# Optimization experiments

Hardware: AMD Instinct MI355X
Metric: run time of the kernel (lower is better)

Reference implementation:

```python
import jax, jax.numpy as jnp
import numpy as np

B, S, HID = 2, 2048, 2048
H, KV, D = 16, 8, 128          # query heads, kv heads, head dim
NREP = H // KV
EPS = 1e-6
THETA = 1000000.0
SCALE = 1.0 / np.sqrt(D)


def setup_inputs() -> dict:
    key = jax.random.key(0)
    ks = jax.random.split(key, 5)
    x = jax.random.normal(ks[0], (B, S, HID), jnp.float32)
    std = 0.02
    Wq = jax.random.normal(ks[1], (HID, H * D), jnp.float32) * std
    Wk = jax.random.normal(ks[2], (HID, KV * D), jnp.float32) * std
    Wv = jax.random.normal(ks[3], (HID, KV * D), jnp.float32) * std
    Wo = jax.random.normal(ks[4], (H * D, HID), jnp.float32) * std
    q_norm_w = jnp.ones((D,), jnp.float32)
    k_norm_w = jnp.ones((D,), jnp.float32)
    # standard RoPE cos/sin table: [S, D]
    inv_freq = 1.0 / (THETA ** (jnp.arange(0, D, 2, dtype=jnp.float32) / D))
    freqs = jnp.arange(S, dtype=jnp.float32)[:, None] * inv_freq[None, :]
    emb = jnp.concatenate([freqs, freqs], axis=-1)
    return {"x": x, "Wq": Wq, "Wk": Wk, "Wv": Wv, "Wo": Wo,
            "q_norm_w": q_norm_w, "k_norm_w": k_norm_w,
            "cos": jnp.cos(emb), "sin": jnp.sin(emb)}


def _rmsnorm(x, w, eps=EPS):
    var = jnp.mean(jnp.square(x), axis=-1, keepdims=True)
    return w * (x * jax.lax.rsqrt(var + eps))


def _rotate_half(x):
    x1, x2 = jnp.split(x, 2, axis=-1)
    return jnp.concatenate([-x2, x1], axis=-1)


def _rope(t, cos, sin):
    # t: [B, h, S, D]; cos/sin: [S, D]
    return t * cos[None, None] + _rotate_half(t) * sin[None, None]


def reference(x, Wq, Wk, Wv, Wo, q_norm_w, k_norm_w, cos, sin):
    q = (x @ Wq).reshape(B, S, H, D)
    k = (x @ Wk).reshape(B, S, KV, D)
    v = (x @ Wv).reshape(B, S, KV, D)
    q = _rmsnorm(q, q_norm_w).transpose(0, 2, 1, 3)   # [B, H, S, D]
    k = _rmsnorm(k, k_norm_w).transpose(0, 2, 1, 3)   # [B, KV, S, D]
    v = v.transpose(0, 2, 1, 3)                       # [B, KV, S, D]
    q = _rope(q, cos, sin)
    k = _rope(k, cos, sin)
    # GQA without materializing repeated K/V: group q heads per kv head
    qg = q.reshape(B, KV, NREP, S, D)
    scores = jnp.einsum('bgrsd,bgtd->bgrst', qg, k) * SCALE  # [B,KV,NREP,S,S]
    causal = jnp.tril(jnp.ones((S, S), dtype=bool))
    scores = jnp.where(causal, scores, jnp.finfo(scores.dtype).min)
    p = jax.nn.softmax(scores, axis=-1)
    out = jnp.einsum('bgrst,bgtd->bgrsd', p, v).reshape(B, H, S, D)
    out = out.transpose(0, 2, 1, 3).reshape(B, S, H * D)
    return out @ Wo
```

## Files before the change

kernel.cpp:

```cpp
#include <hip/hip_runtime.h>

typedef unsigned short u16;
typedef __bf16 bf16x8 __attribute__((ext_vector_type(8)));
typedef float f32x4 __attribute__((ext_vector_type(4)));

#define Bn 2
#define Sn 2048
#define HIDn 2048
#define Hn 16
#define KVn 8
#define Dn 128
#define SCALEf 0.08838834764831845f

__device__ __forceinline__ float b2f(u16 v) {
  return __builtin_bit_cast(float, (unsigned)v << 16);
}
__device__ __forceinline__ u16 f2b(float f) {
  unsigned u = __builtin_bit_cast(unsigned, f);
  u += 0x7fffu + ((u >> 16) & 1u);
  return (u16)(u >> 16);
}
__device__ __forceinline__ bool is_bf16(const void* det) {
  return *(const unsigned*)det == 0x3F803F80u;
}
__device__ __forceinline__ float ldx(const void* p, long i, bool isbf) {
  return isbf ? b2f(((const u16*)p)[i]) : ((const float*)p)[i];
}
__device__ __forceinline__ void gl_lds16(const u16* g, u16* l) {
  __builtin_amdgcn_global_load_lds(
      (unsigned int __attribute__((address_space(1)))*)g,
      (unsigned int __attribute__((address_space(3)))*)l, 16, 0, 0);
}

template <int CTRL>
__device__ __forceinline__ float dpp_mov(float x) {
  return __builtin_bit_cast(
      float, __builtin_amdgcn_update_dpp(0, __builtin_bit_cast(int, x), CTRL,
                                         0xF, 0xF, true));
}
__device__ __forceinline__ float red16_max(float x) {
  x = fmaxf(x, dpp_mov<0xB1>(x));
  x = fmaxf(x, dpp_mov<0x4E>(x));
  x = fmaxf(x, dpp_mov<0x141>(x));
  x = fmaxf(x, dpp_mov<0x140>(x));
  return x;
}
__device__ __forceinline__ float red16_sum(float x) {
  x += dpp_mov<0xB1>(x);
  x += dpp_mov<0x4E>(x);
  x += dpp_mov<0x141>(x);
  x += dpp_mov<0x140>(x);
  return x;
}

__global__ __launch_bounds__(256) void convert_x(
    const void* __restrict__ in, u16* __restrict__ out, const void* __restrict__ det) {
  bool isbf = is_bf16(det);
  long i = ((long)blockIdx.x * 256 + threadIdx.x) * 4;
  if (isbf) {
    *(ushort4*)(out + i) = *(const ushort4*)((const u16*)in + i);
  } else {
    float4 f = *(const float4*)((const float*)in + i);
    out[i] = f2b(f.x); out[i + 1] = f2b(f.y); out[i + 2] = f2b(f.z); out[i + 3] = f2b(f.w);
  }
}

__global__ __launch_bounds__(256) void transpose_any(
    const void* __restrict__ vin, u16* __restrict__ out, const void* __restrict__ det,
    int irs, int ors, long ib0, long ob0, int nb1, long ib1, long ob1) {
  __shared__ u16 tile[64][65];
  bool isbf = det ? is_bf16(det) : true;
  int bz = blockIdx.z;
  long ibase = (long)(bz / nb1) * ib0 + (long)(bz % nb1) * ib1;
  u16* op = out + (long)(bz / nb1) * ob0 + (long)(bz % nb1) * ob1;
  long r0 = (long)blockIdx.y * 64, c0 = (long)blockIdx.x * 64;
  int t = threadIdx.x;
  int tr = t >> 3, tc = (t & 7) * 8;
#pragma unroll
  for (int p = 0; p < 2; ++p) {
    int r = p * 32 + tr;
    long src = ibase + (r0 + r) * irs + c0 + tc;
    if (isbf) {
      const u16* ip = (const u16*)vin;
#pragma unroll
      for (int j = 0; j < 8; ++j) tile[r][tc + j] = ip[src + j];
    } else {
      const float* ip = (const float*)vin;
#pragma unroll
      for (int j = 0; j < 8; ++j) tile[r][tc + j] = f2b(ip[src + j]);
    }
  }
  __syncthreads();
#pragma unroll
  for (int p = 0; p < 2; ++p) {
    int r = p * 32 + tr;
    u16* dst = op + (c0 + r) * ors + r0 + tc;
#pragma unroll
    for (int j = 0; j < 8; ++j) dst[j] = tile[tc + j][r];
  }
}

__global__ __launch_bounds__(256) void gemm_bt(
    const u16* __restrict__ A, const u16* __restrict__ Bt, u16* __restrict__ C,
    float* __restrict__ Cf, const void* __restrict__ det, int N, int K) {
  __shared__ alignas(16) u16 As[128 * 32];
  __shared__ alignas(16) u16 Bs[128 * 32];
  int t = threadIdx.x;
  int wave = t >> 6, lane = t & 63, quad = lane >> 4, l15 = lane & 15;
  long bm = (long)blockIdx.y * 128, bn = (long)blockIdx.x * 128;
  int wm = (wave >> 1) * 64, wn = (wave & 1) * 64;
  f32x4 acc[4][4] = {};
  int sg = ((t & 3) ^ ((t >> 3) & 3)) * 8;
  const u16* Ab = A + (bm + (t >> 2)) * K + sg;
  const u16* Bb = Bt + (bn + (t >> 2)) * K + sg;
  int fg = (quad ^ ((l15 >> 1) & 3)) * 8;
  for (int k0 = 0; k0 < K; k0 += 32) {
    __syncthreads();
    gl_lds16(Ab + k0, As + t * 8);
    gl_lds16(Ab + (long)64 * K + k0, As + 2048 + t * 8);
    gl_lds16(Bb + k0, Bs + t * 8);
    gl_lds16(Bb + (long)64 * K + k0, Bs + 2048 + t * 8);
    __syncthreads();
    bf16x8 a[4], b[4];
#pragma unroll
    for (int i = 0; i < 4; ++i)
      a[i] = *(const bf16x8*)(As + (wm + i * 16 + l15) * 32 + fg);
#pragma unroll
    for (int j = 0; j < 4; ++j)
      b[j] = *(const bf16x8*)(Bs + (wn + j * 16 + l15) * 32 + fg);
#pragma unroll
    for (int i = 0; i < 4; ++i)
#pragma unroll
      for (int j = 0; j < 4; ++j)
        acc[i][j] = __builtin_amdgcn_mfma_f32_16x16x32_bf16(a[i], b[j], acc[i][j], 0, 0, 0);
  }
  bool tofloat = (Cf != nullptr) && !is_bf16(det);
#pragma unroll
  for (int i = 0; i < 4; ++i) {
    long row = bm + wm + i * 16 + quad * 4;
#pragma unroll
    for (int j = 0; j < 4; ++j) {
      long col = bn + wn + j * 16 + l15;
      if (tofloat) {
#pragma unroll
        for (int r = 0; r < 4; ++r) Cf[(row + r) * N + col] = acc[i][j][r];
      } else {
#pragma unroll
        for (int r = 0; r < 4; ++r) C[(row + r) * N + col] = f2b(acc[i][j][r]);
      }
    }
  }
}

__global__ __launch_bounds__(256) void gemm_proj_fused(
    const u16* __restrict__ A, const u16* __restrict__ Bt,
    u16* __restrict__ OutRope, u16* __restrict__ OutPlain, int nrope,
    const void* __restrict__ w, const void* __restrict__ cosb,
    const void* __restrict__ sinb, int K) {
  __shared__ alignas(16) u16 As[128 * 32];
  __shared__ alignas(16) u16 Bs[128 * 32];
  bool isbf = is_bf16(w);
  int t = threadIdx.x;
  int wave = t >> 6, lane = t & 63, quad = lane >> 4, l15 = lane & 15;
  long bm = (long)blockIdx.y * 128;
  int h = blockIdx.x;
  long bn = (long)h * 128;
  int wm = wave * 32;
  f32x4 acc[2][8] = {};
  int sg = ((t & 3) ^ ((t >> 3) & 3)) * 8;
  const u16* Ab = A + (bm + (t >> 2)) * K + sg;
  const u16* Bb = Bt + (bn + (t >> 2)) * K + sg;
  int fg = (quad ^ ((l15 >> 1) & 3)) * 8;
  for (int k0 = 0; k0 < K; k0 += 32) {
    __syncthreads();
    gl_lds16(Ab + k0, As + t * 8);
    gl_lds16(Ab + (long)64 * K + k0, As + 2048 + t * 8);
    gl_lds16(Bb + k0, Bs + t * 8);
    gl_lds16(Bb + (long)64 * K + k0, Bs + 2048 + t * 8);
    __syncthreads();
    bf16x8 a[2], b[8];
#pragma unroll
    for (int i = 0; i < 2; ++i)
      a[i] = *(const bf16x8*)(As + (wm + i * 16 + l15) * 32 + fg);
#pragma unroll
    for (int j = 0; j < 8; ++j)
      b[j] = *(const bf16x8*)(Bs + (j * 16 + l15) * 32 + fg);
#pragma unroll
    for (int i = 0; i < 2; ++i)
#pragma unroll
      for (int j = 0; j < 8; ++j)
        acc[i][j] = __builtin_amdgcn_mfma_f32_16x16x32_bf16(a[i], b[j], acc[i][j], 0, 0, 0);
  }
  if (h < nrope) {
#pragma unroll
    for (int i = 0; i < 2; ++i) {
#pragma unroll
      for (int r = 0; r < 4; ++r) {
        float ss = 0.f;
#pragma unroll
        for (int j = 0; j < 8; ++j) { float v = acc[i][j][r]; ss += v * v; }
        ss = red16_sum(ss);
        float scale = rsqrtf(ss * (1.0f / 128.0f) + 1e-6f);
        int m = (int)bm + wm + i * 16 + quad * 4 + r;
        int b = m >> 11, s = m & (Sn - 1);
        u16* dst = OutRope + (((long)b * nrope + h) * Sn + s) * Dn;
        long cb = (long)s * Dn;
#pragma unroll
        for (int j = 0; j < 4; ++j) {
          int c1i = j * 16 + l15, c2i = c1i + 64;
          float x1 = acc[i][j][r] * scale * ldx(w, c1i, isbf);
          float x2 = acc[i][j + 4][r] * scale * ldx(w, c2i, isbf);
          float c1 = ldx(cosb, cb + c1i, isbf), s1 = ldx(sinb, cb + c1i, isbf);
          float c2 = ldx(cosb, cb + c2i, isbf), s2 = ldx(sinb, cb + c2i, isbf);
          dst[c1i] = f2b(x1 * c1 - x2 * s1);
          dst[c2i] = f2b(x2 * c2 + x1 * s2);
        }
      }
    }
  } else {
    long col0 = (long)(h - nrope) * 128;
#pragma unroll
    for (int i = 0; i < 2; ++i) {
#pragma unroll
      for (int r = 0; r < 4; ++r) {
        long m = bm + wm + i * 16 + quad * 4 + r;
        u16* dst = OutPlain + m * 1024 + col0;
#pragma unroll
        for (int j = 0; j < 8; ++j) dst[j * 16 + l15] = f2b(acc[i][j][r]);
      }
    }
  }
}

__global__ __launch_bounds__(512) void attn_kernel(
    const u16* __restrict__ Qr, const u16* __restrict__ Kr,
    const u16* __restrict__ Vt, u16* __restrict__ Aout) {
  __shared__ alignas(16) u16 Ks[64 * 128];
  __shared__ alignas(16) u16 Vs[128 * 64];
  __shared__ alignas(16) u16 Ps[8][16 * 64];
  int t = threadIdx.x, wave = t >> 6, lane = t & 63, quad = lane >> 4, l15 = lane & 15;
  int bh = blockIdx.y, b = bh >> 4, h = bh & 15, kvh = h >> 1;
  const u16* kbase = Kr + ((long)b * KVn + kvh) * Sn * Dn;
  const u16* vbase = Vt + ((long)b * KVn + kvh) * (long)Dn * Sn;
  int krow = t >> 4;
  int kgr = ((t & 15) ^ (krow & 15)) * 8;
  int vrow = t >> 3;
  int vgr = ((t & 7) ^ (vrow & 7)) * 8;
  u16* ps = (u16*)Ps[wave];

  for (int half = 0; half < 2; ++half) {
    int qt = half == 0 ? (int)blockIdx.x : 15 - (int)blockIdx.x;
    int row0 = qt * 128 + wave * 16;
    const u16* qbase = Qr + (((long)b * Hn + h) * Sn + row0) * Dn;
    bf16x8 aq[4];
#pragma unroll
    for (int kt = 0; kt < 4; ++kt)
      aq[kt] = *(const bf16x8*)(qbase + l15 * Dn + kt * 32 + quad * 8);
    f32x4 o[8] = {};
    float mi[4], li[4];
#pragma unroll
    for (int r = 0; r < 4; ++r) { mi[r] = -1e30f; li[r] = 0.f; }
    int kv_end = qt * 128 + 128;
    for (int kv0 = 0; kv0 < kv_end; kv0 += 64) {
      __syncthreads();
      {
        const u16* kg = kbase + ((long)kv0 + krow) * Dn + kgr;
        gl_lds16(kg, Ks + t * 8);
        gl_lds16(kg + (long)32 * Dn, Ks + 4096 + t * 8);
        const u16* vg = vbase + (long)vrow * Sn + kv0 + vgr;
        gl_lds16(vg, Vs + t * 8);
        gl_lds16(vg + (long)64 * Sn, Vs + 4096 + t * 8);
      }
      __syncthreads();
      if (kv0 <= row0 + 15) {
        f32x4 sc[4] = {};
#pragma unroll
        for (int kt = 0; kt < 4; ++kt) {
          bf16x8 bk[4];
#pragma unroll
          for (int n = 0; n < 4; ++n)
            bk[n] = *(const bf16x8*)(Ks + (n * 16 + l15) * 128 + (((kt * 4 + quad) ^ l15) * 8));
#pragma unroll
          for (int n = 0; n < 4; ++n)
            sc[n] = __builtin_amdgcn_mfma_f32_16x16x32_bf16(aq[kt], bk[n], sc[n], 0, 0, 0);
        }
        f32x4 sv[4];
#pragma unroll
        for (int n = 0; n < 4; ++n)
#pragma unroll
          for (int r = 0; r < 4; ++r) sv[n][r] = sc[n][r] * SCALEf;
        if (kv0 + 63 > row0) {
#pragma unroll
          for (int n = 0; n < 4; ++n) {
            int col = kv0 + n * 16 + l15;
#pragma unroll
            for (int r = 0; r < 4; ++r)
              if (col > row0 + quad * 4 + r) sv[n][r] = -1e30f;
          }
        }
        float alpha[4], pr[4][4];
#pragma unroll
        for (int r = 0; r < 4; ++r) {
          float mx = fmaxf(fmaxf(sv[0][r], sv[1][r]), fmaxf(sv[2][r], sv[3][r]));
          mx = red16_max(mx);
          float mnew = fmaxf(mi[r], mx);
          alpha[r] = __expf(mi[r] - mnew);
          mi[r] = mnew;
          float rs = 0.f;
#pragma unroll
          for (int n = 0; n < 4; ++n) {
            float pv = __expf(sv[n][r] - mnew);
            pr[r][n] = pv;
            rs += pv;
          }
          rs = red16_sum(rs);
          li[r] = li[r] * alpha[r] + rs;
        }
#pragma unroll
        for (int n = 0; n < 8; ++n)
#pragma unroll
          for (int r = 0; r < 4; ++r) o[n][r] *= alpha[r];
#pragma unroll
        for (int n = 0; n < 4; ++n)
#pragma unroll
          for (int r = 0; r < 4; ++r) {
            int prow = quad * 4 + r;
            int pg = (n * 2 + (l15 >> 3)) ^ (prow & 7);
            ps[prow * 64 + pg * 8 + (l15 & 7)] = f2b(pr[r][n]);
          }
#pragma unroll
        for (int kt2 = 0; kt2 < 2; ++kt2) {
          bf16x8 ap = *(const bf16x8*)(ps + l15 * 64 + (((kt2 * 4 + quad) ^ (l15 & 7)) * 8));
#pragma unroll
          for (int n = 0; n < 8; ++n) {
            bf16x8 bv = *(const bf16x8*)(Vs + (n * 16 + l15) * 64 + (((kt2 * 4 + quad) ^ (l15 & 7)) * 8));
            o[n] = __builtin_amdgcn_mfma_f32_16x16x32_bf16(ap, bv, o[n], 0, 0, 0);
          }
        }
      }
    }
#pragma unroll
    for (int r = 0; r < 4; ++r) {
      long s = row0 + quad * 4 + r;
      float inv = 1.0f / li[r];
      u16* dst = Aout + (((long)b * Sn + s) * Hn + h) * Dn;
#pragma unroll
      for (int n = 0; n < 8; ++n) dst[n * 16 + l15] = f2b(o[n][r] * inv);
    }
  }
}

extern "C" void kernel_launch(void* const* d_in, const int* in_sizes, int n_in,
                              void* d_out, int out_size, void* d_ws, size_t ws_size,
                              hipStream_t stream) {
  (void)in_sizes; (void)n_in; (void)out_size; (void)ws_size;
  const void* x    = d_in[0];
  const void* Wq   = d_in[1];
  const void* Wk   = d_in[2];
  const void* Wv   = d_in[3];
  const void* Wo   = d_in[4];
  const void* qw   = d_in[5];
  const void* kw   = d_in[6];
  const void* cosb = d_in[7];
  const void* sinb = d_in[8];
  u16* ws = (u16*)d_ws;
  u16* dsc = (u16*)d_out;

  u16* Qr    = dsc + 0;
  u16* Kr    = dsc + 8388608;
  u16* Wslot = dsc + 12582912;
  u16* Vt    = dsc + 12582912;
  u16* xb   = ws + 0;
  u16* vb   = ws + 8388608;
  u16* attn = ws + 0;
  u16* WoT  = ws + 8388608;

  dim3 blk(256);
  convert_x<<<dim3(8192), blk, 0, stream>>>(x, xb, qw);
  transpose_any<<<dim3(32, 32, 1), blk, 0, stream>>>(Wq, Wslot, qw, 2048, 2048, 0, 0, 1, 0, 0);
  gemm_proj_fused<<<dim3(16, 32), blk, 0, stream>>>(xb, Wslot, Qr, nullptr, Hn, qw, cosb, sinb, 2048);
  transpose_any<<<dim3(16, 32, 1), blk, 0, stream>>>(Wk, Wslot, qw, 1024, 2048, 0, 0, 1, 0, 0);
  transpose_any<<<dim3(16, 32, 1), blk, 0, stream>>>(Wv, Wslot + (long)1024 * 2048, qw, 1024, 2048, 0, 0, 1, 0, 0);
  gemm_proj_fused<<<dim3(16, 32), blk, 0, stream>>>(xb, Wslot, Kr, vb, KVn, kw, cosb, sinb, 2048);
  transpose_any<<<dim3(2, 32, 16), blk, 0, stream>>>(
      vb, Vt, nullptr, KVn * Dn, Sn, 2097152L, 2097152L, KVn, (long)Dn, (long)Dn * Sn);
  attn_kernel<<<dim3(8, 32), dim3(512), 0, stream>>>(Qr, Kr, Vt, attn);
  transpose_any<<<dim3(32, 32, 1), blk, 0, stream>>>(Wo, WoT, qw, 2048, 2048, 0, 0, 1, 0, 0);
  gemm_bt<<<dim3(16, 32), blk, 0, stream>>>(attn, WoT, (u16*)d_out, (float*)d_out, qw, 2048, 2048);
}
```

Baseline: 412.2 us.

## Double-buffer K/V tiles in attention with prefetch, setprio and skip-rescale

The attention kernel now keeps two LDS buffers for K and V and issues the global-to-LDS loads for the next 64-key tile before computing on the current one, so load latency overlaps with MFMA work. It uses one vmcnt wait plus barrier per iteration instead of two syncthreads. It also raises wave priority around MFMA sections and skips rescaling the output accumulator when no row's running max changed. The cost is double the K/V LDS footprint, which may lower occupancy. The barrier placement after compute also needs to be right to avoid a read/write race on the alternate buffer.

```diff
diff --git a/kernel.cpp b/kernel.cpp
--- a/kernel.cpp
+++ b/kernel.cpp
@@ -235,8 +235,8 @@
 __global__ __launch_bounds__(512) void attn_kernel(
     const u16* __restrict__ Qr, const u16* __restrict__ Kr,
     const u16* __restrict__ Vt, u16* __restrict__ Aout) {
-  __shared__ alignas(16) u16 Ks[64 * 128];
-  __shared__ alignas(16) u16 Vs[128 * 64];
+  __shared__ alignas(16) u16 Ks[2][64 * 128];
+  __shared__ alignas(16) u16 Vs[2][128 * 64];
   __shared__ alignas(16) u16 Ps[8][16 * 64];
   int t = threadIdx.x, wave = t >> 6, lane = t & 63, quad = lane >> 4, l15 = lane & 15;
   int bh = blockIdx.y, b = bh >> 4, h = bh & 15, kvh = h >> 1;
@@ -260,30 +260,47 @@
     float mi[4], li[4];
 #pragma unroll
     for (int r = 0; r < 4; ++r) { mi[r] = -1e30f; li[r] = 0.f; }
-    int kv_end = qt * 128 + 128;
-    for (int kv0 = 0; kv0 < kv_end; kv0 += 64) {
-      __syncthreads();
-      {
-        const u16* kg = kbase + ((long)kv0 + krow) * Dn + kgr;
-        gl_lds16(kg, Ks + t * 8);
-        gl_lds16(kg + (long)32 * Dn, Ks + 4096 + t * 8);
-        const u16* vg = vbase + (long)vrow * Sn + kv0 + vgr;
-        gl_lds16(vg, Vs + t * 8);
-        gl_lds16(vg + (long)64 * Sn, Vs + 4096 + t * 8);
+    int nt = (qt * 128 + 128) >> 6;
+    {
+      const u16* kg = kbase + (long)krow * Dn + kgr;
+      gl_lds16(kg, Ks[0] + t * 8);
+      gl_lds16(kg + (long)32 * Dn, Ks[0] + 4096 + t * 8);
+      const u16* vg = vbase + (long)vrow * Sn + vgr;
+      gl_lds16(vg, Vs[0] + t * 8);
+      gl_lds16(vg + (long)64 * Sn, Vs[0] + 4096 + t * 8);
+    }
+    asm volatile("s_waitcnt vmcnt(0)" ::: "memory");
+    __builtin_amdgcn_s_barrier();
+    for (int ti = 0; ti < nt; ++ti) {
+      int kv0 = ti << 6;
+      int cur = ti & 1;
+      if (ti + 1 < nt) {
+        int kn = kv0 + 64;
+        u16* kd = Ks[cur ^ 1];
+        u16* vd = Vs[cur ^ 1];
+        const u16* kg = kbase + ((long)kn + krow) * Dn + kgr;
+        gl_lds16(kg, kd + t * 8);
+        gl_lds16(kg + (long)32 * Dn, kd + 4096 + t * 8);
+        const u16* vg = vbase + (long)vrow * Sn + kn + vgr;
+        gl_lds16(vg, vd + t * 8);
+        gl_lds16(vg + (long)64 * Sn, vd + 4096 + t * 8);
       }
-      __syncthreads();
       if (kv0 <= row0 + 15) {
+        const u16* ksb = Ks[cur];
+        const u16* vsb = Vs[cur];
         f32x4 sc[4] = {};
+        __builtin_amdgcn_s_setprio(1);
 #pragma unroll
         for (int kt = 0; kt < 4; ++kt) {
           bf16x8 bk[4];
 #pragma unroll
           for (int n = 0; n < 4; ++n)
-            bk[n] = *(const bf16x8*)(Ks + (n * 16 + l15) * 128 + (((kt * 4 + quad) ^ l15) * 8));
+            bk[n] = *(const bf16x8*)(ksb + (n * 16 + l15) * 128 + (((kt * 4 + quad) ^ l15) * 8));
 #pragma unroll
           for (int n = 0; n < 4; ++n)
             sc[n] = __builtin_amdgcn_mfma_f32_16x16x32_bf16(aq[kt], bk[n], sc[n], 0, 0, 0);
         }
+        __builtin_amdgcn_s_setprio(0);
         f32x4 sv[4];
 #pragma unroll
         for (int n = 0; n < 4; ++n)
@@ -316,10 +333,14 @@
           rs = red16_sum(rs);
           li[r] = li[r] * alpha[r] + rs;
         }
-#pragma unroll
-        for (int n = 0; n < 8; ++n)
-#pragma unroll
-          for (int r = 0; r < 4; ++r) o[n][r] *= alpha[r];
+        bool nochange = (alpha[0] == 1.f) & (alpha[1] == 1.f) &
+                        (alpha[2] == 1.f) & (alpha[3] == 1.f);
+        if (!__all((int)nochange)) {
+#pragma unroll
+          for (int n = 0; n < 8; ++n)
+#pragma unroll
+            for (int r = 0; r < 4; ++r) o[n][r] *= alpha[r];
+        }
 #pragma unroll
         for (int n = 0; n < 4; ++n)
 #pragma unroll
@@ -328,16 +349,20 @@
             int pg = (n * 2 + (l15 >> 3)) ^ (prow & 7);
             ps[prow * 64 + pg * 8 + (l15 & 7)] = f2b(pr[r][n]);
           }
+        __builtin_amdgcn_s_setprio(1);
 #pragma unroll
         for (int kt2 = 0; kt2 < 2; ++kt2) {
           bf16x8 ap = *(const bf16x8*)(ps + l15 * 64 + (((kt2 * 4 + quad) ^ (l15 & 7)) * 8));
 #pragma unroll
           for (int n = 0; n < 8; ++n) {
-            bf16x8 bv = *(const bf16x8*)(Vs + (n * 16 + l15) * 64 + (((kt2 * 4 + quad) ^ (l15 & 7)) * 8));
+            bf16x8 bv = *(const bf16x8*)(vsb + (n * 16 + l15) * 64 + (((kt2 * 4 + quad) ^ (l15 & 7)) * 8));
             o[n] = __builtin_amdgcn_mfma_f32_16x16x32_bf16(ap, bv, o[n], 0, 0, 0);
           }
         }
+        __builtin_amdgcn_s_setprio(0);
       }
+      asm volatile("s_waitcnt vmcnt(0)" ::: "memory");
+      __builtin_amdgcn_s_barrier();
     }
 #pragma unroll
     for (int r = 0; r < 4; ++r) {
```

Measured after the change: 416.5 us. About the same (+1.0%).

## Double GEMM K-tile to 64 and write V transposed directly from projection epilogue

Applied to the files above, without the earlier changes.

Both GEMM kernels now stage 64-wide K slices in LDS with an 8-way XOR swizzle. This halves the number of barrier pairs per K loop and issues more MFMAs per sync. The fused K/V projection epilogue now writes V directly in the [B,KV,D,S] transposed layout with 4-element vector stores, which removes the separate transpose kernel and its round trip through memory. Vt moves from the output scratch to the workspace. LDS use per block doubles, which may reduce occupancy.

```diff
diff --git a/kernel.cpp b/kernel.cpp
--- a/kernel.cpp
+++ b/kernel.cpp
@@ -103,36 +103,40 @@
 __global__ __launch_bounds__(256) void gemm_bt(
     const u16* __restrict__ A, const u16* __restrict__ Bt, u16* __restrict__ C,
     float* __restrict__ Cf, const void* __restrict__ det, int N, int K) {
-  __shared__ alignas(16) u16 As[128 * 32];
-  __shared__ alignas(16) u16 Bs[128 * 32];
+  __shared__ alignas(16) u16 As[128 * 64];
+  __shared__ alignas(16) u16 Bs[128 * 64];
   int t = threadIdx.x;
   int wave = t >> 6, lane = t & 63, quad = lane >> 4, l15 = lane & 15;
   long bm = (long)blockIdx.y * 128, bn = (long)blockIdx.x * 128;
   int wm = (wave >> 1) * 64, wn = (wave & 1) * 64;
   f32x4 acc[4][4] = {};
-  int sg = ((t & 3) ^ ((t >> 3) & 3)) * 8;
-  const u16* Ab = A + (bm + (t >> 2)) * K + sg;
-  const u16* Bb = Bt + (bn + (t >> 2)) * K + sg;
-  int fg = (quad ^ ((l15 >> 1) & 3)) * 8;
-  for (int k0 = 0; k0 < K; k0 += 32) {
+  int sg = ((t & 7) ^ ((t >> 3) & 7)) * 8;
+  const u16* Ab = A + (bm + (t >> 3)) * K + sg;
+  const u16* Bb = Bt + (bn + (t >> 3)) * K + sg;
+  for (int k0 = 0; k0 < K; k0 += 64) {
     __syncthreads();
-    gl_lds16(Ab + k0, As + t * 8);
-    gl_lds16(Ab + (long)64 * K + k0, As + 2048 + t * 8);
-    gl_lds16(Bb + k0, Bs + t * 8);
-    gl_lds16(Bb + (long)64 * K + k0, Bs + 2048 + t * 8);
+#pragma unroll
+    for (int p = 0; p < 4; ++p) {
+      gl_lds16(Ab + (long)(p * 32) * K + k0, As + p * 2048 + t * 8);
+      gl_lds16(Bb + (long)(p * 32) * K + k0, Bs + p * 2048 + t * 8);
+    }
     __syncthreads();
-    bf16x8 a[4], b[4];
-#pragma unroll
-    for (int i = 0; i < 4; ++i)
-      a[i] = *(const bf16x8*)(As + (wm + i * 16 + l15) * 32 + fg);
-#pragma unroll
-    for (int j = 0; j < 4; ++j)
-      b[j] = *(const bf16x8*)(Bs + (wn + j * 16 + l15) * 32 + fg);
-#pragma unroll
-    for (int i = 0; i < 4; ++i)
+#pragma unroll
+    for (int kt = 0; kt < 2; ++kt) {
+      int fg = ((kt * 4 + quad) ^ (l15 & 7)) * 8;
+      bf16x8 a[4], b[4];
+#pragma unroll
+      for (int i = 0; i < 4; ++i)
+        a[i] = *(const bf16x8*)(As + (wm + i * 16 + l15) * 64 + fg);
 #pragma unroll
       for (int j = 0; j < 4; ++j)
-        acc[i][j] = __builtin_amdgcn_mfma_f32_16x16x32_bf16(a[i], b[j], acc[i][j], 0, 0, 0);
+        b[j] = *(const bf16x8*)(Bs + (wn + j * 16 + l15) * 64 + fg);
+#pragma unroll
+      for (int i = 0; i < 4; ++i)
+#pragma unroll
+        for (int j = 0; j < 4; ++j)
+          acc[i][j] = __builtin_amdgcn_mfma_f32_16x16x32_bf16(a[i], b[j], acc[i][j], 0, 0, 0);
+    }
   }
   bool tofloat = (Cf != nullptr) && !is_bf16(det);
 #pragma unroll
@@ -154,11 +158,11 @@
 
 __global__ __launch_bounds__(256) void gemm_proj_fused(
     const u16* __restrict__ A, const u16* __restrict__ Bt,
-    u16* __restrict__ OutRope, u16* __restrict__ OutPlain, int nrope,
+    u16* __restrict__ OutRope, u16* __restrict__ VtOut, int nrope,
     const void* __restrict__ w, const void* __restrict__ cosb,
     const void* __restrict__ sinb, int K) {
-  __shared__ alignas(16) u16 As[128 * 32];
-  __shared__ alignas(16) u16 Bs[128 * 32];
+  __shared__ alignas(16) u16 As[128 * 64];
+  __shared__ alignas(16) u16 Bs[128 * 64];
   bool isbf = is_bf16(w);
   int t = threadIdx.x;
   int wave = t >> 6, lane = t & 63, quad = lane >> 4, l15 = lane & 15;
@@ -167,29 +171,33 @@
   long bn = (long)h * 128;
   int wm = wave * 32;
   f32x4 acc[2][8] = {};
-  int sg = ((t & 3) ^ ((t >> 3) & 3)) * 8;
-  const u16* Ab = A + (bm + (t >> 2)) * K + sg;
-  const u16* Bb = Bt + (bn + (t >> 2)) * K + sg;
-  int fg = (quad ^ ((l15 >> 1) & 3)) * 8;
-  for (int k0 = 0; k0 < K; k0 += 32) {
+  int sg = ((t & 7) ^ ((t >> 3) & 7)) * 8;
+  const u16* Ab = A + (bm + (t >> 3)) * K + sg;
+  const u16* Bb = Bt + (bn + (t >> 3)) * K + sg;
+  for (int k0 = 0; k0 < K; k0 += 64) {
     __syncthreads();
-    gl_lds16(Ab + k0, As + t * 8);
-    gl_lds16(Ab + (long)64 * K + k0, As + 2048 + t * 8);
-    gl_lds16(Bb + k0, Bs + t * 8);
-    gl_lds16(Bb + (long)64 * K + k0, Bs + 2048 + t * 8);
+#pragma unroll
+    for (int p = 0; p < 4; ++p) {
+      gl_lds16(Ab + (long)(p * 32) * K + k0, As + p * 2048 + t * 8);
+      gl_lds16(Bb + (long)(p * 32) * K + k0, Bs + p * 2048 + t * 8);
+    }
     __syncthreads();
-    bf16x8 a[2], b[8];
-#pragma unroll
-    for (int i = 0; i < 2; ++i)
-      a[i] = *(const bf16x8*)(As + (wm + i * 16 + l15) * 32 + fg);
-#pragma unroll
-    for (int j = 0; j < 8; ++j)
-      b[j] = *(const bf16x8*)(Bs + (j * 16 + l15) * 32 + fg);
-#pragma unroll
-    for (int i = 0; i < 2; ++i)
+#pragma unroll
+    for (int kt = 0; kt < 2; ++kt) {
+      int fg = ((kt * 4 + quad) ^ (l15 & 7)) * 8;
+      bf16x8 a[2], b[8];
+#pragma unroll
+      for (int i = 0; i < 2; ++i)
+        a[i] = *(const bf16x8*)(As + (wm + i * 16 + l15) * 64 + fg);
 #pragma unroll
       for (int j = 0; j < 8; ++j)
-        acc[i][j] = __builtin_amdgcn_mfma_f32_16x16x32_bf16(a[i], b[j], acc[i][j], 0, 0, 0);
+        b[j] = *(const bf16x8*)(Bs + (j * 16 + l15) * 64 + fg);
+#pragma unroll
+      for (int i = 0; i < 2; ++i)
+#pragma unroll
+        for (int j = 0; j < 8; ++j)
+          acc[i][j] = __builtin_amdgcn_mfma_f32_16x16x32_bf16(a[i], b[j], acc[i][j], 0, 0, 0);
+    }
   }
   if (h < nrope) {
 #pragma unroll
@@ -218,15 +226,21 @@
       }
     }
   } else {
-    long col0 = (long)(h - nrope) * 128;
+    int kv = h - nrope;
+    int bidx = (int)(bm >> 11);
+    int srow = ((int)bm & (Sn - 1)) + wm + quad * 4;
 #pragma unroll
     for (int i = 0; i < 2; ++i) {
-#pragma unroll
-      for (int r = 0; r < 4; ++r) {
-        long m = bm + wm + i * 16 + quad * 4 + r;
-        u16* dst = OutPlain + m * 1024 + col0;
-#pragma unroll
-        for (int j = 0; j < 8; ++j) dst[j * 16 + l15] = f2b(acc[i][j][r]);
+      int s0 = srow + i * 16;
+#pragma unroll
+      for (int j = 0; j < 8; ++j) {
+        int d = j * 16 + l15;
+        ushort4 tmp;
+        tmp.x = f2b(acc[i][j][0]);
+        tmp.y = f2b(acc[i][j][1]);
+        tmp.z = f2b(acc[i][j][2]);
+        tmp.w = f2b(acc[i][j][3]);
+        *(ushort4*)(VtOut + (((long)bidx * KVn + kv) * Dn + d) * Sn + s0) = tmp;
       }
     }
   }
@@ -369,9 +383,8 @@
   u16* Qr    = dsc + 0;
   u16* Kr    = dsc + 8388608;
   u16* Wslot = dsc + 12582912;
-  u16* Vt    = dsc + 12582912;
   u16* xb   = ws + 0;
-  u16* vb   = ws + 8388608;
+  u16* Vt   = ws + 8388608;
   u16* attn = ws + 0;
   u16* WoT  = ws + 8388608;
 
@@ -381,9 +394,7 @@
   gemm_proj_fused<<<dim3(16, 32), blk, 0, stream>>>(xb, Wslot, Qr, nullptr, Hn, qw, cosb, sinb, 2048);
   transpose_any<<<dim3(16, 32, 1), blk, 0, stream>>>(Wk, Wslot, qw, 1024, 2048, 0, 0, 1, 0, 0);
   transpose_any<<<dim3(16, 32, 1), blk, 0, stream>>>(Wv, Wslot + (long)1024 * 2048, qw, 1024, 2048, 0, 0, 1, 0, 0);
-  gemm_proj_fused<<<dim3(16, 32), blk, 0, stream>>>(xb, Wslot, Kr, vb, KVn, kw, cosb, sinb, 2048);
-  transpose_any<<<dim3(2, 32, 16), blk, 0, stream>>>(
-      vb, Vt, nullptr, KVn * Dn, Sn, 2097152L, 2097152L, KVn, (long)Dn, (long)Dn * Sn);
+  gemm_proj_fused<<<dim3(16, 32), blk, 0, stream>>>(xb, Wslot, Kr, Vt, KVn, kw, cosb, sinb, 2048);
   attn_kernel<<<dim3(8, 32), dim3(512), 0, stream>>>(Qr, Kr, Vt, attn);
   transpose_any<<<dim3(32, 32, 1), blk, 0, stream>>>(Wo, WoT, qw, 2048, 2048, 0, 0, 1, 0, 0);
   gemm_bt<<<dim3(16, 32), blk, 0, stream>>>(attn, WoT, (u16*)d_out, (float*)d_out, qw, 2048, 2048);
```

Result: faster. 383.5 us (-7.0%).
